# Optimization experiments

Measured on AMD Instinct MI355X. Metric: run time of the kernel, lower is better.

Reference implementation:

```python
import jax, jax.numpy as jnp
import numpy as np

D_MODEL = 1024
N_HEADS = 16
HEAD_DIM = D_MODEL // N_HEADS


def setup_inputs() -> dict:
    key = jax.random.key(0)
    k1, k2, k3 = jax.random.split(key, 3)
    B, T, C = 4, 2048, D_MODEL
    x = jax.random.normal(k1, (B, T, C), dtype=jnp.float32)
    # torch Linear weight is (out,in); store as (in,out) so y = x @ W
    w_qkv = jax.random.normal(k2, (C, 3 * C), dtype=jnp.float32) * (1.0 / np.sqrt(C))
    w_proj = jax.random.normal(k3, (C, C), dtype=jnp.float32) * (1.0 / np.sqrt(C))
    return {"x": x, "w_qkv": w_qkv, "w_proj": w_proj}


def reference(x, w_qkv, w_proj):
    B, T, C = x.shape
    H, Dh = N_HEADS, HEAD_DIM
    qkv = x @ w_qkv                        # (B,T,3C)
    q, k, v = jnp.split(qkv, 3, axis=-1)
    def heads(t):
        return t.reshape(B, T, H, Dh).transpose(0, 2, 1, 3)  # (B,H,T,Dh)
    q, k, v = heads(q), heads(k), heads(v)
    scores = jnp.einsum('bhqd,bhkd->bhqk', q, k) / np.sqrt(Dh).astype(np.float32)
    causal = jnp.tril(jnp.ones((T, T), dtype=bool))
    scores = jnp.where(causal, scores, -jnp.inf)
    attn = jax.nn.softmax(scores, axis=-1)
    y = jnp.einsum('bhqk,bhkd->bhqd', attn, v)  # (B,H,T,Dh)
    y = y.transpose(0, 2, 1, 3).reshape(B, T, C)
    return y @ w_proj
```

## Files before the change

### kernel.cpp

```cpp
#include <hip/hip_runtime.h>

#define SEQ_T 2048
#define NBATCH 4
#define CDIM 1024
#define NHEAD 16
#define MROWS 8192
#define QKVC 3072

typedef unsigned short u16;
typedef __bf16 bf16x8 __attribute__((ext_vector_type(8)));
typedef float f32x4 __attribute__((ext_vector_type(4)));
typedef unsigned short u16x8 __attribute__((ext_vector_type(8)));
typedef unsigned uint32x4 __attribute__((ext_vector_type(4)));

__device__ __forceinline__ u16 f32_to_bf16(float f) {
  union { float f; unsigned int u; } v; v.f = f;
  unsigned int u = v.u;
  unsigned int r = ((u >> 16) & 1u) + 0x7fffu;
  return (u16)((u + r) >> 16);
}

__device__ __forceinline__ void gload_lds16(const u16* g, u16* l) {
  __builtin_amdgcn_global_load_lds(
      (const __attribute__((address_space(1))) void*)g,
      (__attribute__((address_space(3))) void*)l, 16, 0, 0);
}


__global__ __launch_bounds__(256) void cast_block_kernel(const float* __restrict__ in,
                                                         u16* __restrict__ out) {
  const int i = blockIdx.x * 256 + threadIdx.x;
  const int kg = i & 127;
  const int row = i >> 7;
  const float4 v0 = ((const float4*)in)[i * 2];
  const float4 v1 = ((const float4*)in)[i * 2 + 1];
  union { u16 u[8]; bf16x8 b; } o;
  o.u[0] = f32_to_bf16(v0.x); o.u[1] = f32_to_bf16(v0.y);
  o.u[2] = f32_to_bf16(v0.z); o.u[3] = f32_to_bf16(v0.w);
  o.u[4] = f32_to_bf16(v1.x); o.u[5] = f32_to_bf16(v1.y);
  o.u[6] = f32_to_bf16(v1.z); o.u[7] = f32_to_bf16(v1.w);
  const int tile = (row >> 4) * 32 + (kg >> 2);
  const int lane = (row & 15) + ((kg & 3) << 4);
  *(bf16x8*)(out + (size_t)tile * 512 + lane * 8) = o.b;
}

__global__ void transpose_cast_block_kernel(const float* __restrict__ in,
                                            u16* __restrict__ out, int Cc) {
  __shared__ float tile[32][33];
  const int c0 = blockIdx.x * 32, r0 = blockIdx.y * 32;
  const int tx = threadIdx.x, ty = threadIdx.y;
  #pragma unroll
  for (int i = 0; i < 32; i += 8)
    tile[ty + i][tx] = in[(size_t)(r0 + ty + i) * Cc + c0 + tx];
  __syncthreads();
  const int t = ty * 32 + tx;
  if (t < 128) {
    const int cc = t & 31, kgq = t >> 5;
    union { u16 u[8]; bf16x8 b; } o;
    #pragma unroll
    for (int j = 0; j < 8; ++j) o.u[j] = f32_to_bf16(tile[kgq * 8 + j][cc]);
    const int rowN = c0 + cc;
    const int tileI = (rowN >> 4) * 32 + (r0 >> 5);
    const int lane = (rowN & 15) + (kgq << 4);
    *(bf16x8*)(out + (size_t)tileI * 512 + lane * 8) = o.b;
  }
}

__global__ __launch_bounds__(256, 3)
void gemm1_kernel(const u16* __restrict__ Ab, const u16* __restrict__ Bb,
                  u16* __restrict__ Qb, u16* __restrict__ Kc, u16* __restrict__ Vc) {
  __shared__ u16 lds[24576];
  const int tid = threadIdx.x;
  const int lane = tid & 63, w = tid >> 6;
  const int wm = w >> 1, wn = w & 1;
  const int l15 = lane & 15, lhi = lane >> 4;
  const int row0 = blockIdx.x * 128, col0 = blockIdx.y * 128;
  const int rt0 = row0 >> 4, ct0 = col0 >> 4;

  const u16* aT = Ab + (size_t)(rt0 + w * 2) * 16384 + lane * 8;
  const u16* bT = Bb + (size_t)(ct0 + w * 2) * 16384 + lane * 8;

  f32x4 acc[4][4] = {};

#define SA(S) (lds + (S) * 4096)
#define SB(S) (lds + 12288 + (S) * 4096)
#define STAGE(KT, S)                                                            \
  {                                                                             \
    gload_lds16(aT + (size_t)(KT) * 512,         SA(S) + (w * 2) * 512);        \
    gload_lds16(aT + 16384 + (size_t)(KT) * 512, SA(S) + (w * 2 + 1) * 512);    \
    gload_lds16(bT + (size_t)(KT) * 512,         SB(S) + (w * 2) * 512);        \
    gload_lds16(bT + 16384 + (size_t)(KT) * 512, SB(S) + (w * 2 + 1) * 512);    \
  }
#define COMPUTE(S)                                                              \
  {                                                                             \
    bf16x8 af[4], bf[4];                                                        \
    _Pragma("unroll") for (int mi = 0; mi < 4; ++mi)                            \
      af[mi] = *(const bf16x8*)(SA(S) + (wm * 4 + mi) * 512 + lane * 8);        \
    _Pragma("unroll") for (int ni = 0; ni < 4; ++ni)                            \
      bf[ni] = *(const bf16x8*)(SB(S) + (wn * 4 + ni) * 512 + lane * 8);        \
    __builtin_amdgcn_s_setprio(1);                                              \
    _Pragma("unroll") for (int mi = 0; mi < 4; ++mi)                            \
      _Pragma("unroll") for (int ni = 0; ni < 4; ++ni)                          \
        acc[mi][ni] = __builtin_amdgcn_mfma_f32_16x16x32_bf16(af[mi], bf[ni],   \
                                                              acc[mi][ni], 0, 0, 0); \
    __builtin_amdgcn_s_setprio(0);                                              \
  }
#define WAITBAR4                                                                \
  asm volatile("s_waitcnt vmcnt(4)" ::: "memory");                              \
  __builtin_amdgcn_sched_barrier(0);                                            \
  __builtin_amdgcn_s_barrier();

  STAGE(0, 0);
  STAGE(1, 1);
  WAITBAR4;

  #pragma unroll 1
  for (int kt = 0; kt < 30; kt += 3) {
    STAGE(kt + 2, 2); COMPUTE(0); WAITBAR4;
    STAGE(kt + 3, 0); COMPUTE(1); WAITBAR4;
    STAGE(kt + 4, 1); COMPUTE(2); WAITBAR4;
  }
  COMPUTE(0);
  asm volatile("s_waitcnt vmcnt(0)" ::: "memory");
  __builtin_amdgcn_sched_barrier(0);
  __builtin_amdgcn_s_barrier();
  COMPUTE(1);
#undef STAGE
#undef COMPUTE
#undef WAITBAR4
#undef SA
#undef SB

  const int region = col0 >> 10;
  if (region == 0) {
    #pragma unroll
    for (int mt = 0; mt < 4; ++mt)
      #pragma unroll
      for (int nt = 0; nt < 4; ++nt)
        #pragma unroll
        for (int r = 0; r < 4; ++r) {
          const int rr = row0 + wm * 64 + mt * 16 + lhi * 4 + r;
          const int cc = col0 + wn * 64 + nt * 16 + l15;
          Qb[(size_t)rr * CDIM + cc] = f32_to_bf16(acc[mt][nt][r] * 0.18033688011f);
        }
  } else {
    __syncthreads();
    if (region == 1) {
      #pragma unroll
      for (int mt = 0; mt < 4; ++mt)
        #pragma unroll
        for (int nt = 0; nt < 4; ++nt)
          #pragma unroll
          for (int r = 0; r < 4; ++r) {
            const int sidx = (wn * 4 + wm * 2 + (mt >> 1)) * 2048
                           + ((mt & 1) * 2 + (nt >> 1)) * 512
                           + ((nt & 1) * 2 + (l15 >> 3)) * 128
                           + (lhi * 4 + r) * 8 + (l15 & 7);
            lds[sidx] = f32_to_bf16(acc[mt][nt][r]);
          }
    } else {
      #pragma unroll
      for (int mt = 0; mt < 4; ++mt)
        #pragma unroll
        for (int nt = 0; nt < 4; ++nt)
          #pragma unroll
          for (int r = 0; r < 4; ++r) {
            const int sidx = (wn * 4 + wm * 2 + (mt >> 1)) * 2048
                           + nt * 512
                           + ((mt & 1) * 2 + (lhi >> 1)) * 128
                           + l15 * 8 + (lhi & 1) * 4 + r;
            lds[sidx] = f32_to_bf16(acc[mt][nt][r]);
          }
    }
    __syncthreads();
    u16* dstB = (region == 1) ? Kc : Vc;
    const int bb = row0 >> 11;
    const int kv0b = (row0 & 2047) >> 5;
    const int hbase = (col0 & 1023) >> 6;
    #pragma unroll
    for (int hh = 0; hh < 2; ++hh) {
      u16* dst = dstB + (size_t)(bb * 16 + hbase + hh) * 131072 + (size_t)kv0b * 2048;
      const u16* src = lds + hh * 8192;
      #pragma unroll
      for (int c = 0; c < 4; ++c) {
        const int o = (c * 256 + tid) * 8;
        *(uint32x4*)(dst + o) = *(const uint32x4*)(src + o);
      }
    }
  }
}

__global__ __launch_bounds__(256, 3)
void gemm2_kernel(const u16* __restrict__ Ab, const u16* __restrict__ Bb,
                  float* __restrict__ C) {
  __shared__ u16 lds[24576];
  const int tid = threadIdx.x;
  const int lane = tid & 63, w = tid >> 6;
  const int wm = w >> 1, wn = w & 1;
  const int l15 = lane & 15, lhi = lane >> 4;
  const int row0 = blockIdx.x * 128, col0 = blockIdx.y * 128;
  const int rt0 = row0 >> 4, ct0 = col0 >> 4;

  const u16* aT = Ab + (size_t)(rt0 + w * 2) * 16384 + lane * 8;
  const u16* bT = Bb + (size_t)(ct0 + w * 2) * 16384 + lane * 8;

  f32x4 acc[4][4] = {};

#define SA(S) (lds + (S) * 4096)
#define SB(S) (lds + 12288 + (S) * 4096)
#define STAGE(KT, S)                                                            \
  {                                                                             \
    gload_lds16(aT + (size_t)(KT) * 512,         SA(S) + (w * 2) * 512);        \
    gload_lds16(aT + 16384 + (size_t)(KT) * 512, SA(S) + (w * 2 + 1) * 512);    \
    gload_lds16(bT + (size_t)(KT) * 512,         SB(S) + (w * 2) * 512);        \
    gload_lds16(bT + 16384 + (size_t)(KT) * 512, SB(S) + (w * 2 + 1) * 512);    \
  }
#define COMPUTE(S)                                                              \
  {                                                                             \
    bf16x8 af[4], bf[4];                                                        \
    _Pragma("unroll") for (int mi = 0; mi < 4; ++mi)                            \
      af[mi] = *(const bf16x8*)(SA(S) + (wm * 4 + mi) * 512 + lane * 8);        \
    _Pragma("unroll") for (int ni = 0; ni < 4; ++ni)                            \
      bf[ni] = *(const bf16x8*)(SB(S) + (wn * 4 + ni) * 512 + lane * 8);        \
    __builtin_amdgcn_s_setprio(1);                                              \
    _Pragma("unroll") for (int mi = 0; mi < 4; ++mi)                            \
      _Pragma("unroll") for (int ni = 0; ni < 4; ++ni)                          \
        acc[mi][ni] = __builtin_amdgcn_mfma_f32_16x16x32_bf16(af[mi], bf[ni],   \
                                                              acc[mi][ni], 0, 0, 0); \
    __builtin_amdgcn_s_setprio(0);                                              \
  }
#define WAITBAR4                                                                \
  asm volatile("s_waitcnt vmcnt(4)" ::: "memory");                              \
  __builtin_amdgcn_sched_barrier(0);                                            \
  __builtin_amdgcn_s_barrier();

  STAGE(0, 0);
  STAGE(1, 1);
  WAITBAR4;

  #pragma unroll 1
  for (int kt = 0; kt < 30; kt += 3) {
    STAGE(kt + 2, 2); COMPUTE(0); WAITBAR4;
    STAGE(kt + 3, 0); COMPUTE(1); WAITBAR4;
    STAGE(kt + 4, 1); COMPUTE(2); WAITBAR4;
  }
  COMPUTE(0);
  asm volatile("s_waitcnt vmcnt(0)" ::: "memory");
  __builtin_amdgcn_sched_barrier(0);
  __builtin_amdgcn_s_barrier();
  COMPUTE(1);
#undef STAGE
#undef COMPUTE
#undef WAITBAR4
#undef SA
#undef SB

  #pragma unroll
  for (int mt = 0; mt < 4; ++mt)
    #pragma unroll
    for (int nt = 0; nt < 4; ++nt)
      #pragma unroll
      for (int r = 0; r < 4; ++r) {
        const int rr = row0 + wm * 64 + mt * 16 + lhi * 4 + r;
        const int cc = col0 + wn * 64 + nt * 16 + l15;
        C[(size_t)rr * CDIM + cc] = acc[mt][nt][r];
      }
}

template <bool DOMASK>
__device__ __forceinline__ void attn_step(const bf16x8 (&qf)[2],
                                          const bf16x8 (&kf)[2][2],
                                          const bf16x8 (&vb)[4],
                                          const bf16x8 ones,
                                          f32x4 (&acc)[4], f32x4& acc1,
                                          int l15, int lhi, int kv0, int qg) {
  f32x4 st[2];
  #pragma unroll
  for (int t = 0; t < 2; ++t) {
    f32x4 z = {0.f, 0.f, 0.f, 0.f};
    z = __builtin_amdgcn_mfma_f32_16x16x32_bf16(kf[t][0], qf[0], z, 0, 0, 0);
    z = __builtin_amdgcn_mfma_f32_16x16x32_bf16(kf[t][1], qf[1], z, 0, 0, 0);
    st[t] = z;
  }
  #pragma unroll
  for (int t = 0; t < 2; ++t)
    #pragma unroll
    for (int r = 0; r < 4; ++r) {
      float sv = st[t][r];
      if (DOMASK) {
        const int kvg = kv0 + t * 16 + lhi * 4 + r;
        sv = (kvg > qg) ? -__builtin_inff() : sv;
      }
      st[t][r] = exp2f(sv);
    }
  unsigned c00, c01, c10, c11;
  asm("v_cvt_pk_bf16_f32 %0, %1, %2" : "=v"(c00) : "v"(st[0][0]), "v"(st[0][1]));
  asm("v_cvt_pk_bf16_f32 %0, %1, %2" : "=v"(c01) : "v"(st[0][2]), "v"(st[0][3]));
  asm("v_cvt_pk_bf16_f32 %0, %1, %2" : "=v"(c10) : "v"(st[1][0]), "v"(st[1][1]));
  asm("v_cvt_pk_bf16_f32 %0, %1, %2" : "=v"(c11) : "v"(st[1][2]), "v"(st[1][3]));
  asm("v_permlane32_swap_b32 %0, %1" : "+v"(c00), "+v"(c10));
  asm("v_permlane32_swap_b32 %0, %1" : "+v"(c01), "+v"(c11));
  asm("v_permlane16_swap_b32 %0, %1" : "+v"(c00), "+v"(c10));
  asm("v_permlane16_swap_b32 %0, %1" : "+v"(c01), "+v"(c11));
  uint32x4 pw; pw[0] = c00; pw[1] = c01; pw[2] = c10; pw[3] = c11;
  const bf16x8 pa = __builtin_bit_cast(bf16x8, pw);
  #pragma unroll
  for (int d = 0; d < 4; ++d)
    acc[d] = __builtin_amdgcn_mfma_f32_16x16x32_bf16(pa, vb[d], acc[d], 0, 0, 0);
  acc1 = __builtin_amdgcn_mfma_f32_16x16x32_bf16(pa, ones, acc1, 0, 0, 0);
}

__global__ __launch_bounds__(256, 4) void attn_kernel(const u16* __restrict__ Qb,
                                                      const u16* __restrict__ Kc,
                                                      const u16* __restrict__ Vc,
                                                      u16* __restrict__ Yb) {
  __shared__ u16 Kl[2][4096];
  __shared__ u16 Vl[2][4096];
  const int tid = threadIdx.x, lane = tid & 63, wid = tid >> 6;
  const int l15 = lane & 15, lhi = lane >> 4;
  const int id = blockIdx.x;
  const int xcd = id & 7, k = (id >> 3) & 15, hi3 = id >> 7;
  const int bh = hi3 * 8 + xcd;
  const int b = bh >> 4, h = bh & 15;
  const int pa = k * 4 + wid;
  const int qA0 = pa * 16, qB0 = (127 - pa) * 16;
  const int nchA = pa / 2 + 1, nchB = (127 - pa) / 2 + 1;
  const int nc2max = 32 - k;
  const u16* Qp  = Qb + (size_t)b * SEQ_T * CDIM + h * 64;
  const u16* KcC = Kc + (size_t)bh * 131072;
  const u16* VcC = Vc + (size_t)bh * 131072;

  u16x8 ou;
  #pragma unroll
  for (int j = 0; j < 8; ++j) ou[j] = 0x3F80;
  const bf16x8 ones = __builtin_bit_cast(bf16x8, ou);

  gload_lds16(KcC + wid * 512 + lane * 8,        &Kl[0][wid * 512]);
  gload_lds16(KcC + 2048 + wid * 512 + lane * 8, &Kl[0][2048 + wid * 512]);
  gload_lds16(VcC + wid * 512 + lane * 8,        &Vl[0][wid * 512]);
  gload_lds16(VcC + 2048 + wid * 512 + lane * 8, &Vl[0][2048 + wid * 512]);

  bf16x8 qfA[2], qfB[2];
  #pragma unroll
  for (int i = 0; i < 2; ++i) {
    qfA[i] = *(const bf16x8*)(Qp + (size_t)(qA0 + l15) * CDIM + i * 32 + lhi * 8);
    qfB[i] = *(const bf16x8*)(Qp + (size_t)(qB0 + l15) * CDIM + i * 32 + lhi * 8);
  }
  const int qgA = qA0 + l15, qgB = qB0 + l15;

  f32x4 accA[4] = {}, accB[4] = {};
  f32x4 acc1A = {}, acc1B = {};

  __syncthreads();

  int cbuf = 0;
  for (int ic2 = 0; ic2 < nc2max; ++ic2) {
    if (ic2 + 1 < nc2max) {
      const u16* kg = KcC + (size_t)(ic2 + 1) * 4096 + wid * 512 + lane * 8;
      const u16* vg = VcC + (size_t)(ic2 + 1) * 4096 + wid * 512 + lane * 8;
      gload_lds16(kg,        &Kl[cbuf ^ 1][wid * 512]);
      gload_lds16(kg + 2048, &Kl[cbuf ^ 1][2048 + wid * 512]);
      gload_lds16(vg,        &Vl[cbuf ^ 1][wid * 512]);
      gload_lds16(vg + 2048, &Vl[cbuf ^ 1][2048 + wid * 512]);
    }
    #pragma unroll
    for (int h2 = 0; h2 < 2; ++h2) {
      const int c = ic2 * 2 + h2;
      const u16* kb = &Kl[cbuf][h2 * 2048];
      const u16* vp = &Vl[cbuf][h2 * 2048];
      bf16x8 kf[2][2], vb[4];
      #pragma unroll
      for (int t = 0; t < 2; ++t)
        #pragma unroll
        for (int i = 0; i < 2; ++i)
          kf[t][i] = *(const bf16x8*)(kb + (t * 2 + i) * 512 + lane * 8);
      #pragma unroll
      for (int d = 0; d < 4; ++d)
        vb[d] = *(const bf16x8*)(vp + d * 512 + lane * 8);

      const int kv0 = c * 32;
      if (c < nchB) {
        if (c == nchB - 1)
          attn_step<true>(qfB, kf, vb, ones, accB, acc1B, l15, lhi, kv0, qgB);
        else
          attn_step<false>(qfB, kf, vb, ones, accB, acc1B, l15, lhi, kv0, qgB);
      }
      if (c < nchA) {
        if (c == nchA - 1)
          attn_step<true>(qfA, kf, vb, ones, accA, acc1A, l15, lhi, kv0, qgA);
        else
          attn_step<false>(qfA, kf, vb, ones, accA, acc1A, l15, lhi, kv0, qgA);
      }
    }
    __syncthreads();
    cbuf ^= 1;
  }

  #pragma unroll
  for (int r = 0; r < 4; ++r) {
    const float ivA = 1.0f / acc1A[r];
    const float ivB = 1.0f / acc1B[r];
    const int rl = lhi * 4 + r;
    #pragma unroll
    for (int d = 0; d < 4; ++d) {
      const int lofs = (rl + (((d * 2 + (l15 >> 3)) & 3) << 4)) * 8 + (l15 & 7);
      Yb[((size_t)(b * 128 + pa)        * 32 + h * 2 + (d >> 1)) * 512 + lofs] =
          f32_to_bf16(accA[d][r] * ivA);
      Yb[((size_t)(b * 128 + (127 - pa)) * 32 + h * 2 + (d >> 1)) * 512 + lofs] =
          f32_to_bf16(accB[d][r] * ivB);
    }
  }
}

extern "C" void kernel_launch(void* const* d_in, const int* in_sizes, int n_in,
                              void* d_out, int out_size, void* d_ws, size_t ws_size,
                              hipStream_t stream) {
  const float* x      = (const float*)d_in[0];
  const float* w_qkv  = (const float*)d_in[1];
  const float* w_proj = (const float*)d_in[2];
  float* out = (float*)d_out;

  u16* Xb  = (u16*)d_ws;
  u16* Wqt = Xb  + (size_t)MROWS * CDIM;
  u16* Wpt = Wqt + (size_t)QKVC * CDIM;
  u16* Qb  = Wpt + (size_t)CDIM * CDIM;
  u16* Kc  = Qb  + (size_t)MROWS * CDIM;
  u16* Vc  = Kc  + (size_t)64 * 131072;
  u16* Yb  = Vc  + (size_t)64 * 131072;

  cast_block_kernel<<<MROWS * CDIM / 8 / 256, 256, 0, stream>>>(x, Xb);
  transpose_cast_block_kernel<<<dim3(QKVC / 32, CDIM / 32), dim3(32, 8), 0, stream>>>(w_qkv, Wqt, QKVC);
  transpose_cast_block_kernel<<<dim3(CDIM / 32, CDIM / 32), dim3(32, 8), 0, stream>>>(w_proj, Wpt, CDIM);

  gemm1_kernel<<<dim3(MROWS / 128, QKVC / 128), 256, 0, stream>>>(Xb, Wqt, Qb, Kc, Vc);

  attn_kernel<<<1024, 256, 0, stream>>>(Qb, Kc, Vc, Yb);

  gemm2_kernel<<<dim3(MROWS / 128, CDIM / 128), 256, 0, stream>>>(Yb, Wpt, out);
}
```

Baseline: 156.1 us.

## Switch attention to 32x32x16 MFMA tiles with 32-row query blocks

```diff
diff --git a/kernel.cpp b/kernel.cpp
--- a/kernel.cpp
+++ b/kernel.cpp
@@ -10,6 +10,7 @@
 typedef unsigned short u16;
 typedef __bf16 bf16x8 __attribute__((ext_vector_type(8)));
 typedef float f32x4 __attribute__((ext_vector_type(4)));
+typedef float f32x16 __attribute__((ext_vector_type(16)));
 typedef unsigned short u16x8 __attribute__((ext_vector_type(8)));
 typedef unsigned uint32x4 __attribute__((ext_vector_type(4)));
 
@@ -152,10 +153,10 @@
         for (int nt = 0; nt < 4; ++nt)
           #pragma unroll
           for (int r = 0; r < 4; ++r) {
-            const int sidx = (wn * 4 + wm * 2 + (mt >> 1)) * 2048
-                           + ((mt & 1) * 2 + (nt >> 1)) * 512
-                           + ((nt & 1) * 2 + (l15 >> 3)) * 128
-                           + (lhi * 4 + r) * 8 + (l15 & 7);
+            const int sidx = wn * 8192 + (wm * 2 + (mt >> 1)) * 2048
+                           + nt * 512
+                           + ((mt & 1) * 16 + lhi * 4 + r + ((l15 >> 3) & 1) * 32) * 8
+                           + (l15 & 7);
             lds[sidx] = f32_to_bf16(acc[mt][nt][r]);
           }
     } else {
@@ -165,10 +166,10 @@
         for (int nt = 0; nt < 4; ++nt)
           #pragma unroll
           for (int r = 0; r < 4; ++r) {
-            const int sidx = (wn * 4 + wm * 2 + (mt >> 1)) * 2048
-                           + nt * 512
-                           + ((mt & 1) * 2 + (lhi >> 1)) * 128
-                           + l15 * 8 + (lhi & 1) * 4 + r;
+            const int sidx = wn * 8192 + (wm * 2 + (mt >> 1)) * 2048
+                           + ((mt & 1) * 2 + (nt >> 1)) * 512
+                           + ((nt & 1) * 16 + l15 + 32 * (lhi >> 1)) * 8
+                           + (lhi & 1) * 4 + r;
             lds[sidx] = f32_to_bf16(acc[mt][nt][r]);
           }
     }
@@ -268,64 +269,68 @@
 }
 
 template <bool DOMASK>
-__device__ __forceinline__ void attn_step(const bf16x8 (&qf)[2],
-                                          const bf16x8 (&kf)[2][2],
-                                          const bf16x8 (&vb)[4],
-                                          const bf16x8 ones,
-                                          f32x4 (&acc)[4], f32x4& acc1,
-                                          int l15, int lhi, int kv0, int qg) {
-  f32x4 st[2];
-  #pragma unroll
-  for (int t = 0; t < 2; ++t) {
-    f32x4 z = {0.f, 0.f, 0.f, 0.f};
-    z = __builtin_amdgcn_mfma_f32_16x16x32_bf16(kf[t][0], qf[0], z, 0, 0, 0);
-    z = __builtin_amdgcn_mfma_f32_16x16x32_bf16(kf[t][1], qf[1], z, 0, 0, 0);
-    st[t] = z;
-  }
-  #pragma unroll
-  for (int t = 0; t < 2; ++t)
-    #pragma unroll
-    for (int r = 0; r < 4; ++r) {
-      float sv = st[t][r];
-      if (DOMASK) {
-        const int kvg = kv0 + t * 16 + lhi * 4 + r;
-        sv = (kvg > qg) ? -__builtin_inff() : sv;
-      }
-      st[t][r] = exp2f(sv);
-    }
-  unsigned c00, c01, c10, c11;
-  asm("v_cvt_pk_bf16_f32 %0, %1, %2" : "=v"(c00) : "v"(st[0][0]), "v"(st[0][1]));
-  asm("v_cvt_pk_bf16_f32 %0, %1, %2" : "=v"(c01) : "v"(st[0][2]), "v"(st[0][3]));
-  asm("v_cvt_pk_bf16_f32 %0, %1, %2" : "=v"(c10) : "v"(st[1][0]), "v"(st[1][1]));
-  asm("v_cvt_pk_bf16_f32 %0, %1, %2" : "=v"(c11) : "v"(st[1][2]), "v"(st[1][3]));
-  asm("v_permlane32_swap_b32 %0, %1" : "+v"(c00), "+v"(c10));
-  asm("v_permlane32_swap_b32 %0, %1" : "+v"(c01), "+v"(c11));
-  asm("v_permlane16_swap_b32 %0, %1" : "+v"(c00), "+v"(c10));
-  asm("v_permlane16_swap_b32 %0, %1" : "+v"(c01), "+v"(c11));
-  uint32x4 pw; pw[0] = c00; pw[1] = c01; pw[2] = c10; pw[3] = c11;
-  const bf16x8 pa = __builtin_bit_cast(bf16x8, pw);
-  #pragma unroll
-  for (int d = 0; d < 4; ++d)
-    acc[d] = __builtin_amdgcn_mfma_f32_16x16x32_bf16(pa, vb[d], acc[d], 0, 0, 0);
-  acc1 = __builtin_amdgcn_mfma_f32_16x16x32_bf16(pa, ones, acc1, 0, 0, 0);
-}
-
-__global__ __launch_bounds__(256, 4) void attn_kernel(const u16* __restrict__ Qb,
+__device__ __forceinline__ void attn_step32(const bf16x8 (&qf)[4],
+                                            const bf16x8 (&kf)[4],
+                                            const bf16x8 (&vb)[2][2],
+                                            const bf16x8 ones,
+                                            f32x16 (&acc)[2], f32x16& acc1,
+                                            int l31, int lhi5, int kv0, int qg) {
+  f32x16 st = {};
+  #pragma unroll
+  for (int i = 0; i < 4; ++i)
+    st = __builtin_amdgcn_mfma_f32_32x32x16_bf16(kf[i], qf[i], st, 0, 0, 0);
+  #pragma unroll
+  for (int g = 0; g < 16; ++g) {
+    float sv = st[g];
+    if (DOMASK) {
+      const int kvg = kv0 + (g & 3) + 8 * (g >> 2) + 4 * lhi5;
+      sv = (kvg > qg) ? -__builtin_inff() : sv;
+    }
+    st[g] = exp2f(sv);
+  }
+  unsigned c0, c1, c2, c3, c4, c5, c6, c7;
+  asm("v_cvt_pk_bf16_f32 %0, %1, %2" : "=v"(c0) : "v"(st[0]),  "v"(st[1]));
+  asm("v_cvt_pk_bf16_f32 %0, %1, %2" : "=v"(c1) : "v"(st[2]),  "v"(st[3]));
+  asm("v_cvt_pk_bf16_f32 %0, %1, %2" : "=v"(c2) : "v"(st[4]),  "v"(st[5]));
+  asm("v_cvt_pk_bf16_f32 %0, %1, %2" : "=v"(c3) : "v"(st[6]),  "v"(st[7]));
+  asm("v_cvt_pk_bf16_f32 %0, %1, %2" : "=v"(c4) : "v"(st[8]),  "v"(st[9]));
+  asm("v_cvt_pk_bf16_f32 %0, %1, %2" : "=v"(c5) : "v"(st[10]), "v"(st[11]));
+  asm("v_cvt_pk_bf16_f32 %0, %1, %2" : "=v"(c6) : "v"(st[12]), "v"(st[13]));
+  asm("v_cvt_pk_bf16_f32 %0, %1, %2" : "=v"(c7) : "v"(st[14]), "v"(st[15]));
+  asm("v_permlane32_swap_b32 %0, %1" : "+v"(c0), "+v"(c2));
+  asm("v_permlane32_swap_b32 %0, %1" : "+v"(c1), "+v"(c3));
+  asm("v_permlane32_swap_b32 %0, %1" : "+v"(c4), "+v"(c6));
+  asm("v_permlane32_swap_b32 %0, %1" : "+v"(c5), "+v"(c7));
+  uint32x4 p0w, p1w;
+  p0w[0] = c0; p0w[1] = c1; p0w[2] = c2; p0w[3] = c3;
+  p1w[0] = c4; p1w[1] = c5; p1w[2] = c6; p1w[3] = c7;
+  const bf16x8 pa0 = __builtin_bit_cast(bf16x8, p0w);
+  const bf16x8 pa1 = __builtin_bit_cast(bf16x8, p1w);
+  acc[0] = __builtin_amdgcn_mfma_f32_32x32x16_bf16(pa0, vb[0][0], acc[0], 0, 0, 0);
+  acc[0] = __builtin_amdgcn_mfma_f32_32x32x16_bf16(pa1, vb[1][0], acc[0], 0, 0, 0);
+  acc[1] = __builtin_amdgcn_mfma_f32_32x32x16_bf16(pa0, vb[0][1], acc[1], 0, 0, 0);
+  acc[1] = __builtin_amdgcn_mfma_f32_32x32x16_bf16(pa1, vb[1][1], acc[1], 0, 0, 0);
+  acc1 = __builtin_amdgcn_mfma_f32_32x32x16_bf16(pa0, ones, acc1, 0, 0, 0);
+  acc1 = __builtin_amdgcn_mfma_f32_32x32x16_bf16(pa1, ones, acc1, 0, 0, 0);
+}
+
+__global__ __launch_bounds__(256, 2) void attn_kernel(const u16* __restrict__ Qb,
                                                       const u16* __restrict__ Kc,
                                                       const u16* __restrict__ Vc,
                                                       u16* __restrict__ Yb) {
   __shared__ u16 Kl[2][4096];
   __shared__ u16 Vl[2][4096];
   const int tid = threadIdx.x, lane = tid & 63, wid = tid >> 6;
-  const int l15 = lane & 15, lhi = lane >> 4;
+  const int l31 = lane & 31, lhi5 = lane >> 5;
   const int id = blockIdx.x;
-  const int xcd = id & 7, k = (id >> 3) & 15, hi3 = id >> 7;
+  const int xcd = id & 7, graw = (id >> 3) & 7, hi3 = id >> 6;
+  const int g = (hi3 & 4) ? (7 - graw) : graw;
   const int bh = hi3 * 8 + xcd;
   const int b = bh >> 4, h = bh & 15;
-  const int pa = k * 4 + wid;
-  const int qA0 = pa * 16, qB0 = (127 - pa) * 16;
-  const int nchA = pa / 2 + 1, nchB = (127 - pa) / 2 + 1;
-  const int nc2max = 32 - k;
+  const int pa = g * 4 + wid;
+  const int qA0 = pa * 32, qB0 = (63 - pa) * 32;
+  const int nchA = pa + 1, nchB = 64 - pa;
+  const int nc2max = 32 - 2 * g;
   const u16* Qp  = Qb + (size_t)b * SEQ_T * CDIM + h * 64;
   const u16* KcC = Kc + (size_t)bh * 131072;
   const u16* VcC = Vc + (size_t)bh * 131072;
@@ -340,16 +345,16 @@
   gload_lds16(VcC + wid * 512 + lane * 8,        &Vl[0][wid * 512]);
   gload_lds16(VcC + 2048 + wid * 512 + lane * 8, &Vl[0][2048 + wid * 512]);
 
-  bf16x8 qfA[2], qfB[2];
-  #pragma unroll
-  for (int i = 0; i < 2; ++i) {
-    qfA[i] = *(const bf16x8*)(Qp + (size_t)(qA0 + l15) * CDIM + i * 32 + lhi * 8);
-    qfB[i] = *(const bf16x8*)(Qp + (size_t)(qB0 + l15) * CDIM + i * 32 + lhi * 8);
-  }
-  const int qgA = qA0 + l15, qgB = qB0 + l15;
-
-  f32x4 accA[4] = {}, accB[4] = {};
-  f32x4 acc1A = {}, acc1B = {};
+  bf16x8 qfA[4], qfB[4];
+  #pragma unroll
+  for (int i = 0; i < 4; ++i) {
+    qfA[i] = *(const bf16x8*)(Qp + (size_t)(qA0 + l31) * CDIM + i * 16 + lhi5 * 8);
+    qfB[i] = *(const bf16x8*)(Qp + (size_t)(qB0 + l31) * CDIM + i * 16 + lhi5 * 8);
+  }
+  const int qgA = qA0 + l31, qgB = qB0 + l31;
+
+  f32x16 accA[2] = {}, accB[2] = {};
+  f32x16 acc1A = {}, acc1B = {};
 
   __syncthreads();
 
@@ -368,28 +373,28 @@
       const int c = ic2 * 2 + h2;
       const u16* kb = &Kl[cbuf][h2 * 2048];
       const u16* vp = &Vl[cbuf][h2 * 2048];
-      bf16x8 kf[2][2], vb[4];
-      #pragma unroll
-      for (int t = 0; t < 2; ++t)
+      bf16x8 kf[4], vb[2][2];
+      #pragma unroll
+      for (int i = 0; i < 4; ++i)
+        kf[i] = *(const bf16x8*)(kb + i * 512 + lane * 8);
+      #pragma unroll
+      for (int kk = 0; kk < 2; ++kk)
         #pragma unroll
-        for (int i = 0; i < 2; ++i)
-          kf[t][i] = *(const bf16x8*)(kb + (t * 2 + i) * 512 + lane * 8);
-      #pragma unroll
-      for (int d = 0; d < 4; ++d)
-        vb[d] = *(const bf16x8*)(vp + d * 512 + lane * 8);
+        for (int dh = 0; dh < 2; ++dh)
+          vb[kk][dh] = *(const bf16x8*)(vp + (kk * 2 + dh) * 512 + lane * 8);
 
       const int kv0 = c * 32;
       if (c < nchB) {
         if (c == nchB - 1)
-          attn_step<true>(qfB, kf, vb, ones, accB, acc1B, l15, lhi, kv0, qgB);
+          attn_step32<true>(qfB, kf, vb, ones, accB, acc1B, l31, lhi5, kv0, qgB);
         else
-          attn_step<false>(qfB, kf, vb, ones, accB, acc1B, l15, lhi, kv0, qgB);
+          attn_step32<false>(qfB, kf, vb, ones, accB, acc1B, l31, lhi5, kv0, qgB);
       }
       if (c < nchA) {
         if (c == nchA - 1)
-          attn_step<true>(qfA, kf, vb, ones, accA, acc1A, l15, lhi, kv0, qgA);
+          attn_step32<true>(qfA, kf, vb, ones, accA, acc1A, l31, lhi5, kv0, qgA);
         else
-          attn_step<false>(qfA, kf, vb, ones, accA, acc1A, l15, lhi, kv0, qgA);
+          attn_step32<false>(qfA, kf, vb, ones, accA, acc1A, l31, lhi5, kv0, qgA);
       }
     }
     __syncthreads();
@@ -397,17 +402,22 @@
   }
 
   #pragma unroll
-  for (int r = 0; r < 4; ++r) {
-    const float ivA = 1.0f / acc1A[r];
-    const float ivB = 1.0f / acc1B[r];
-    const int rl = lhi * 4 + r;
-    #pragma unroll
-    for (int d = 0; d < 4; ++d) {
-      const int lofs = (rl + (((d * 2 + (l15 >> 3)) & 3) << 4)) * 8 + (l15 & 7);
-      Yb[((size_t)(b * 128 + pa)        * 32 + h * 2 + (d >> 1)) * 512 + lofs] =
-          f32_to_bf16(accA[d][r] * ivA);
-      Yb[((size_t)(b * 128 + (127 - pa)) * 32 + h * 2 + (d >> 1)) * 512 + lofs] =
-          f32_to_bf16(accB[d][r] * ivB);
+  for (int g2 = 0; g2 < 16; ++g2) {
+    const int qlA = (g2 & 3) + 8 * (g2 >> 2) + 4 * lhi5;
+    const float ivA = 1.0f / acc1A[g2];
+    const float ivB = 1.0f / acc1B[g2];
+    const int laneb = ((qlA & 15)) + ((l31 >> 3) << 4);
+    const int jj = l31 & 7;
+    #pragma unroll
+    for (int dh = 0; dh < 2; ++dh) {
+      const int qA = qA0 + qlA;
+      const int qB = qB0 + qlA;
+      const size_t rrA = (size_t)b * 2048 + qA;
+      const size_t rrB = (size_t)b * 2048 + qB;
+      Yb[((rrA >> 4) * 32 + h * 2 + dh) * 512 + laneb * 8 + jj] =
+          f32_to_bf16(accA[dh][g2] * ivA);
+      Yb[((rrB >> 4) * 32 + h * 2 + dh) * 512 + laneb * 8 + jj] =
+          f32_to_bf16(accB[dh][g2] * ivB);
     }
   }
 }
@@ -434,7 +444,7 @@
 
   gemm1_kernel<<<dim3(MROWS / 128, QKVC / 128), 256, 0, stream>>>(Xb, Wqt, Qb, Kc, Vc);
 
-  attn_kernel<<<1024, 256, 0, stream>>>(Qb, Kc, Vc, Yb);
+  attn_kernel<<<512, 256, 0, stream>>>(Qb, Kc, Vc, Yb);
 
   gemm2_kernel<<<dim3(MROWS / 128, CDIM / 128), 256, 0, stream>>>(Yb, Wpt, out);
 }
```

Measured after the change: 158.9 us. No clear change (+1.8%).
